# Kernel optimization log

Hardware: AMD Instinct MI355X
Metric: run time of the kernel (lower is better)

The kernel has to match this reference:

```python
import jax, jax.numpy as jnp
import numpy as np

B, N, D, DEG = 64, 128, 64, 16  # graphs, nodes/graph, emb_dim, degree


def setup_inputs() -> dict:
    key = jax.random.key(0)
    k1, k2 = jax.random.split(key)
    # ring-lattice edges per graph: node i -> (i+k) % N, k=1..DEG (no self loops, no duplicates)
    src_local = jnp.repeat(jnp.arange(N, dtype=jnp.int32), DEG)            # [N*DEG]
    dst_local = (src_local + jnp.tile(jnp.arange(1, DEG + 1, dtype=jnp.int32), N)) % N
    offsets = (jnp.arange(B, dtype=jnp.int32) * N)[:, None]                 # [B,1]
    src = (src_local[None, :] + offsets).reshape(-1)                        # [B*N*DEG]
    dst = (dst_local[None, :] + offsets).reshape(-1)
    edge_index = jnp.stack([src, dst], axis=0)                              # [2, E]
    batch_vec = jnp.repeat(jnp.arange(B, dtype=jnp.int32), N)               # [B*N]
    edge_attr = jax.random.normal(k1, (B * N * DEG, D), dtype=jnp.float32)
    emb_table = jax.random.normal(k2, (3, D), dtype=jnp.float32)
    emb_table = emb_table.at[0].set(0.0)  # padding_idx=0 -> zero row
    return {"edge_attr": edge_attr, "emb_table": emb_table,
            "edge_index": edge_index, "batch_vec": batch_vec,
            "num_graphs": B, "max_nodes": N}


def reference(edge_attr, emb_table, edge_index, batch_vec, num_graphs, max_nodes):
    total_nodes = batch_vec.shape[0]
    ones = jnp.ones((total_nodes,), dtype=jnp.int32)
    counts = jax.ops.segment_sum(ones, batch_vec, num_segments=num_graphs)  # nodes per graph
    offsets = jnp.cumsum(counts) - counts                                   # exclusive cumsum
    local = jnp.arange(total_nodes, dtype=jnp.int32) - offsets[batch_vec]   # node idx within graph

    g = batch_vec[edge_index[0]]            # graph id per edge
    si = local[edge_index[0]]
    di = local[edge_index[1]]

    # to_dense_adj(edge_index, batch, edge_attr): scatter-add edge features -> [B, N, N, D]
    edge_dense = jnp.zeros((num_graphs, max_nodes, max_nodes, edge_attr.shape[-1]),
                           dtype=edge_attr.dtype)
    edge_dense = edge_dense.at[g, si, di].add(edge_attr)

    # A = 2 - dense(edge val 2, self-loop val 1, else 0) -> 0 edge, 1 diag, 2 disconnected/pad
    A = jnp.full((num_graphs, max_nodes, max_nodes), 2, dtype=jnp.int32)
    A = A.at[g, si, di].add(-2)
    A = A.at[batch_vec, local, local].add(-1)

    # Embedding(3, D, padding_idx=0): row 0 is zeros
    emb = emb_table[A] * (A != 0)[..., None].astype(emb_table.dtype)
    return edge_dense + emb
```

## Files before the change

kernel.cpp:

```cpp
#include <hip/hip_runtime.h>


__global__ void prep_kernel(const int* __restrict__ batch, int* __restrict__ ws,
                            int TN, int B) {
    extern __shared__ int cnt[];
    for (int i = threadIdx.x; i < B; i += blockDim.x) cnt[i] = 0;
    __syncthreads();
    for (int v = threadIdx.x; v < TN; v += blockDim.x)
        atomicAdd(&cnt[batch[v]], 1);
    __syncthreads();
    if (threadIdx.x == 0) {
        int acc = 0;
        for (int g = 0; g < B; ++g) {
            int c = cnt[g];
            ws[g]     = acc;
            ws[B + g] = c;
            acc += c;
        }
    }
}

__global__ void fill_kernel(float4* __restrict__ out, const float4* __restrict__ emb,
                            const int* __restrict__ counts, int N, int D4, int jPer) {
    int g  = blockIdx.z;
    int i  = blockIdx.y;
    int d4 = threadIdx.x % D4;
    int jj = threadIdx.x / D4;
    int j  = blockIdx.x * jPer + jj;
    if (j >= N) return;
    float4 v1 = emb[D4 + d4];
    float4 v2 = emb[2 * D4 + d4];
    bool diag = (j == i) && (i < counts[g]);
    float4 v = diag ? v1 : v2;
    size_t row = (size_t)(g * N + i);
    out[(row * N + j) * D4 + d4] = v;
}

__global__ void edge_kernel(const float4* __restrict__ attr, const int* __restrict__ eidx,
                            const int* __restrict__ batch, const int* __restrict__ offs,
                            float4* __restrict__ out, int E, int N, int D4) {
    int idx = blockIdx.x * blockDim.x + threadIdx.x;
    if (idx >= E * D4) return;
    int e  = idx / D4;
    int d4 = idx - e * D4;
    int s  = eidx[e];
    int d  = eidx[E + e];
    int g  = batch[s];
    int off = offs[g];
    int si = s - off;
    int di = d - off;
    float4 v = attr[(size_t)e * D4 + d4];
    out[(((size_t)g * N + si) * N + di) * D4 + d4] = v;
}

extern "C" void kernel_launch(void* const* d_in, const int* in_sizes, int n_in,
                              void* d_out, int out_size, void* d_ws, size_t ws_size,
                              hipStream_t stream) {
    const float* edge_attr  = (const float*)d_in[0];
    const float* emb_table  = (const float*)d_in[1];
    const int*   edge_index = (const int*)d_in[2];
    const int*   batch_vec  = (const int*)d_in[3];

    int D  = in_sizes[1] / 3;
    int E  = in_sizes[2] / 2;
    int TN = in_sizes[3];
    int D4 = D / 4;
    int N  = (int)((long long)out_size / ((long long)TN * (long long)D));
    int B  = TN / N;

    float* out = (float*)d_out;
    int*   ws  = (int*)d_ws;

    prep_kernel<<<1, 1024, (size_t)B * sizeof(int), stream>>>(batch_vec, ws, TN, B);

    int jPer = 256 / D4;
    dim3 fgrid((N + jPer - 1) / jPer, N, B);
    fill_kernel<<<fgrid, 256, 0, stream>>>((float4*)out, (const float4*)emb_table,
                                           ws + B, N, D4, jPer);

    long long eunits = (long long)E * D4;
    int eblocks = (int)((eunits + 255) / 256);
    edge_kernel<<<eblocks, 256, 0, stream>>>((const float4*)edge_attr, edge_index,
                                             batch_vec, ws, (float4*)out, E, N, D4);
}
```

Baseline: 70.21 us.

## Fuse background fill and edge scatter per row using CSR edge lists

After: 150.2 us. 2.14x slower.

```diff
diff --git a/kernel.cpp b/kernel.cpp
--- a/kernel.cpp
+++ b/kernel.cpp
@@ -1,4 +1,119 @@
 #include <hip/hip_runtime.h>
+
+
+
+__global__ void zero_kernel(int* __restrict__ ws, int beg, int end) {
+    int i = beg + blockIdx.x * blockDim.x + threadIdx.x;
+    int stride = gridDim.x * blockDim.x;
+    for (; i < end; i += stride) ws[i] = 0;
+}
+
+__global__ void hist_kernel(const int* __restrict__ batch, const int* __restrict__ eidx,
+                            int* __restrict__ ws, int B, int TN, int E) {
+    int* counts = ws + B;
+    int* rowcnt = ws + 2 * B + TN + 1;
+    int idx = blockIdx.x * blockDim.x + threadIdx.x;
+    int stride = gridDim.x * blockDim.x;
+    for (int v = idx; v < TN; v += stride) atomicAdd(&counts[batch[v]], 1);
+    for (int e = idx; e < E; e += stride) atomicAdd(&rowcnt[eidx[e]], 1);
+}
+
+__global__ __launch_bounds__(1024) void scan_kernel(int* __restrict__ ws, int B, int TN) {
+    int* offs   = ws;
+    int* counts = ws + B;
+    int* rowoff = ws + 2 * B;
+    int* rowcnt = ws + 2 * B + TN + 1;
+    __shared__ int part[1024];
+    int tid = threadIdx.x;
+    int nb  = (int)blockDim.x;
+    int chunk = (TN + nb - 1) / nb;
+    int s0 = tid * chunk;
+    int s1 = min(s0 + chunk, TN);
+    int sum = 0;
+    for (int r = s0; r < s1; ++r) sum += rowcnt[r];
+    part[tid] = sum;
+    __syncthreads();
+    for (int off = 1; off < nb; off <<= 1) {
+        int v = (tid >= off) ? part[tid - off] : 0;
+        __syncthreads();
+        if (tid >= off) part[tid] += v;
+        __syncthreads();
+    }
+    int excl = (tid == 0) ? 0 : part[tid - 1];
+    for (int r = s0; r < s1; ++r) { rowoff[r] = excl; excl += rowcnt[r]; }
+    if (s1 == TN) rowoff[TN] = excl;
+    if (tid == 0) {
+        int acc = 0;
+        for (int g = 0; g < B; ++g) { offs[g] = acc; acc += counts[g]; }
+    }
+}
+
+__global__ void scatter_kernel(const int* __restrict__ eidx, int* __restrict__ ws,
+                               int2* __restrict__ elist, int B, int TN, int E) {
+    const int* rowoff = ws + 2 * B;
+    int* rowcur = ws + 2 * B + 2 * TN + 1;
+    int idx = blockIdx.x * blockDim.x + threadIdx.x;
+    int stride = gridDim.x * blockDim.x;
+    for (int e = idx; e < E; e += stride) {
+        int s = eidx[e];
+        int pos = atomicAdd(&rowcur[s], 1);
+        elist[rowoff[s] + pos] = make_int2(eidx[E + e], e);
+    }
+}
+
+
+__global__ __launch_bounds__(256) void fused_kernel(
+        const float4* __restrict__ attr, const float4* __restrict__ emb,
+        const int2* __restrict__ elist, const int* __restrict__ ws,
+        float4* __restrict__ out, int B, int N, int D4, int lg) {
+    const int* offs   = ws;
+    const int* counts = ws + B;
+    const int* rowoff = ws + 2 * B;
+
+    int bid = blockIdx.x;
+    int g = bid / N;
+    int i = bid - g * N;
+    int cnt = counts[g];
+    int off = offs[g];
+    bool real = (i < cnt);
+    int kbeg = 0, kend = 0;
+    if (real) {
+        int s = off + i;
+        kbeg = rowoff[s];
+        kend = rowoff[s + 1];
+    }
+    int k = kend - kbeg;
+    if (k > 1024) k = 1024;
+
+    __shared__ int2 lds[1024];
+    for (int m = threadIdx.x; m < k; m += blockDim.x) {
+        int2 v = elist[kbeg + m];
+        lds[m] = make_int2(v.x - off, v.y);
+    }
+    __syncthreads();
+
+    int d4 = threadIdx.x & (D4 - 1);
+    int j0 = threadIdx.x >> lg;
+    int jStep = (int)blockDim.x >> lg;
+    float4 v1 = emb[D4 + d4];
+    float4 v2 = emb[2 * D4 + d4];
+    size_t outBase = (size_t)bid * ((size_t)N << lg);
+
+    for (int j = j0; j < N; j += jStep) {
+        float4 val = (real && j == i) ? v1 : v2;
+        out[outBase + ((size_t)j << lg) + d4] = val;
+    }
+    __syncthreads();
+
+    int units = k << lg;
+    for (int t = threadIdx.x; t < units; t += blockDim.x) {
+        int m  = t >> lg;
+        int dd = t & (D4 - 1);
+        int2 ed = lds[m];
+        float4 a = attr[((size_t)ed.y << lg) + dd];
+        out[outBase + ((size_t)ed.x << lg) + dd] = a;
+    }
+}
 
 
 __global__ void prep_kernel(const int* __restrict__ batch, int* __restrict__ ws,
@@ -13,9 +128,7 @@
         int acc = 0;
         for (int g = 0; g < B; ++g) {
             int c = cnt[g];
-            ws[g]     = acc;
-            ws[B + g] = c;
-            acc += c;
+            ws[g] = acc; ws[B + g] = c; acc += c;
         }
     }
 }
@@ -47,10 +160,8 @@
     int d  = eidx[E + e];
     int g  = batch[s];
     int off = offs[g];
-    int si = s - off;
-    int di = d - off;
-    float4 v = attr[(size_t)e * D4 + d4];
-    out[(((size_t)g * N + si) * N + di) * D4 + d4] = v;
+    out[(((size_t)g * N + (s - off)) * N + (d - off)) * D4 + d4] =
+        attr[(size_t)e * D4 + d4];
 }
 
 extern "C" void kernel_launch(void* const* d_in, const int* in_sizes, int n_in,
@@ -68,18 +179,37 @@
     int N  = (int)((long long)out_size / ((long long)TN * (long long)D));
     int B  = TN / N;
 
+    int lg = 0;
+    while ((1 << lg) < D4) ++lg;
+    bool pow2 = ((1 << lg) == D4) && (D4 >= 1) && (D4 <= 256) && (D % 4 == 0);
+
     float* out = (float*)d_out;
     int*   ws  = (int*)d_ws;
 
-    prep_kernel<<<1, 1024, (size_t)B * sizeof(int), stream>>>(batch_vec, ws, TN, B);
-
-    int jPer = 256 / D4;
-    dim3 fgrid((N + jPer - 1) / jPer, N, B);
-    fill_kernel<<<fgrid, 256, 0, stream>>>((float4*)out, (const float4*)emb_table,
-                                           ws + B, N, D4, jPer);
-
-    long long eunits = (long long)E * D4;
-    int eblocks = (int)((eunits + 255) / 256);
-    edge_kernel<<<eblocks, 256, 0, stream>>>((const float4*)edge_attr, edge_index,
-                                             batch_vec, ws, (float4*)out, E, N, D4);
-}
+    long long intHdr = 2LL * B + 3LL * TN + 1;
+    long long eoffInt = (intHdr + 1) & ~1LL;
+    long long needBytes = eoffInt * 4 + (long long)E * 8;
+
+    if (pow2 && (long long)ws_size >= needBytes) {
+        int2* elist = (int2*)(ws + eoffInt);
+        int zEnd = (int)intHdr;
+
+        zero_kernel<<<64, 256, 0, stream>>>(ws, B, zEnd);
+        hist_kernel<<<256, 256, 0, stream>>>(batch_vec, edge_index, ws, B, TN, E);
+        scan_kernel<<<1, 1024, 0, stream>>>(ws, B, TN);
+        scatter_kernel<<<256, 256, 0, stream>>>(edge_index, ws, elist, B, TN, E);
+        fused_kernel<<<B * N, 256, 0, stream>>>((const float4*)edge_attr,
+                                                (const float4*)emb_table, elist, ws,
+                                                (float4*)out, B, N, D4, lg);
+    } else {
+        prep_kernel<<<1, 1024, (size_t)B * sizeof(int), stream>>>(batch_vec, ws, TN, B);
+        int jPer = 256 / D4;
+        dim3 fgrid((N + jPer - 1) / jPer, N, B);
+        fill_kernel<<<fgrid, 256, 0, stream>>>((float4*)out, (const float4*)emb_table,
+                                               ws + B, N, D4, jPer);
+        long long eunits = (long long)E * D4;
+        int eblocks = (int)((eunits + 255) / 256);
+        edge_kernel<<<eblocks, 256, 0, stream>>>((const float4*)edge_attr, edge_index,
+                                                 batch_vec, ws, (float4*)out, E, N, D4);
+    }
+}
```

## Build edge bitmask to skip overwritten fill stores and merge fill with edge scatter

Applied to the files above, without the earlier changes.

New measurement: 75.43 us. 7.4% more time.

```diff
diff --git a/kernel.cpp b/kernel.cpp
--- a/kernel.cpp
+++ b/kernel.cpp
@@ -1,4 +1,81 @@
 #include <hip/hip_runtime.h>
+
+
+typedef float f4 __attribute__((ext_vector_type(4)));
+
+__global__ __launch_bounds__(256) void prep_zero_kernel(
+        const int* __restrict__ batch, int* __restrict__ offs,
+        f4* __restrict__ mask4, long long mask4N, int TN, int B) {
+    if (blockIdx.x == 0) {
+        __shared__ int cnt[1024];
+        for (int i = threadIdx.x; i < B; i += 256) cnt[i] = 0;
+        __syncthreads();
+        for (int v = threadIdx.x; v < TN; v += 256)
+            atomicAdd(&cnt[batch[v]], 1);
+        __syncthreads();
+        if (threadIdx.x == 0) {
+            int acc = 0;
+            for (int g = 0; g < B; ++g) { offs[g] = acc; acc += cnt[g]; }
+            offs[B] = acc;
+        }
+    } else {
+        long long idx = (long long)(blockIdx.x - 1) * 256 + threadIdx.x;
+        long long stride = (long long)(gridDim.x - 1) * 256;
+        f4 z = {0.f, 0.f, 0.f, 0.f};
+        for (; idx < mask4N; idx += stride) mask4[idx] = z;
+    }
+}
+
+__global__ void mask_build_kernel(const int* __restrict__ eidx,
+                                  const int* __restrict__ batch,
+                                  const int* __restrict__ offs,
+                                  unsigned* __restrict__ mask,
+                                  int E, int N, int lgN) {
+    int e = blockIdx.x * blockDim.x + threadIdx.x;
+    if (e >= E) return;
+    int s = eidx[e], d = eidx[E + e];
+    int g = batch[s];
+    int off = offs[g];
+    long long cell = (((long long)g << lgN) + (s - off)) * N + (d - off);
+    atomicOr(&mask[cell >> 5], 1u << ((int)cell & 31));
+}
+
+__global__ __launch_bounds__(256) void main_kernel(
+        const f4* __restrict__ attr, const f4* __restrict__ emb,
+        const int* __restrict__ eidx, const int* __restrict__ batch,
+        const int* __restrict__ offs, const unsigned* __restrict__ mask,
+        f4* __restrict__ out,
+        int E, int N, int D4, int lg, int lgN, int lgCPR, int eBlocks) {
+    int bid = blockIdx.x;
+    if (bid < eBlocks) {
+        long long idx = (long long)bid * 256 + threadIdx.x;
+        if (idx < ((long long)E << lg)) {
+            int e  = (int)(idx >> lg);
+            int d4 = (int)idx & (D4 - 1);
+            int s = eidx[e], d = eidx[E + e];
+            int g = batch[s];
+            int off = offs[g];
+            size_t row = ((size_t)g << lgN) + (s - off);
+            out[(row * N + (d - off)) * D4 + d4] = attr[((size_t)e << lg) + d4];
+        }
+    } else {
+        int fb   = bid - eBlocks;
+        int chunk = fb & ((1 << lgCPR) - 1);
+        int rowi  = fb >> lgCPR;
+        int i = rowi & (N - 1);
+        int g = rowi >> lgN;
+        int o0 = offs[g], o1 = offs[g + 1];
+        bool real = (i < o1 - o0);
+        int unit = (chunk << 8) + threadIdx.x;
+        int j  = unit >> lg;
+        int d4 = unit & (D4 - 1);
+        f4 v = (real && j == i) ? emb[D4 + d4] : emb[2 * D4 + d4];
+        long long cell = ((long long)rowi << lgN) + j;
+        unsigned bit = (mask[cell >> 5] >> ((int)cell & 31)) & 1u;
+        if (!bit)
+            out[((size_t)rowi << (lgN + lg)) + unit] = v;
+    }
+}
 
 
 __global__ void prep_kernel(const int* __restrict__ batch, int* __restrict__ ws,
@@ -13,14 +90,12 @@
         int acc = 0;
         for (int g = 0; g < B; ++g) {
             int c = cnt[g];
-            ws[g]     = acc;
-            ws[B + g] = c;
-            acc += c;
+            ws[g] = acc; ws[B + g] = c; acc += c;
         }
     }
 }
 
-__global__ void fill_kernel(float4* __restrict__ out, const float4* __restrict__ emb,
+__global__ void fill_kernel(f4* __restrict__ out, const f4* __restrict__ emb,
                             const int* __restrict__ counts, int N, int D4, int jPer) {
     int g  = blockIdx.z;
     int i  = blockIdx.y;
@@ -28,17 +103,17 @@
     int jj = threadIdx.x / D4;
     int j  = blockIdx.x * jPer + jj;
     if (j >= N) return;
-    float4 v1 = emb[D4 + d4];
-    float4 v2 = emb[2 * D4 + d4];
+    f4 v1 = emb[D4 + d4];
+    f4 v2 = emb[2 * D4 + d4];
     bool diag = (j == i) && (i < counts[g]);
-    float4 v = diag ? v1 : v2;
+    f4 v = diag ? v1 : v2;
     size_t row = (size_t)(g * N + i);
     out[(row * N + j) * D4 + d4] = v;
 }
 
-__global__ void edge_kernel(const float4* __restrict__ attr, const int* __restrict__ eidx,
+__global__ void edge_kernel(const f4* __restrict__ attr, const int* __restrict__ eidx,
                             const int* __restrict__ batch, const int* __restrict__ offs,
-                            float4* __restrict__ out, int E, int N, int D4) {
+                            f4* __restrict__ out, int E, int N, int D4) {
     int idx = blockIdx.x * blockDim.x + threadIdx.x;
     if (idx >= E * D4) return;
     int e  = idx / D4;
@@ -47,10 +122,8 @@
     int d  = eidx[E + e];
     int g  = batch[s];
     int off = offs[g];
-    int si = s - off;
-    int di = d - off;
-    float4 v = attr[(size_t)e * D4 + d4];
-    out[(((size_t)g * N + si) * N + di) * D4 + d4] = v;
+    out[(((size_t)g * N + (s - off)) * N + (d - off)) * D4 + d4] =
+        attr[(size_t)e * D4 + d4];
 }
 
 extern "C" void kernel_launch(void* const* d_in, const int* in_sizes, int n_in,
@@ -68,18 +141,51 @@
     int N  = (int)((long long)out_size / ((long long)TN * (long long)D));
     int B  = TN / N;
 
-    float* out = (float*)d_out;
-    int*   ws  = (int*)d_ws;
+    f4*  out = (f4*)d_out;
+    int* ws  = (int*)d_ws;
 
-    prep_kernel<<<1, 1024, (size_t)B * sizeof(int), stream>>>(batch_vec, ws, TN, B);
+    auto ispow2 = [](int x) { return x > 0 && (x & (x - 1)) == 0; };
+    int lg = 0;  while ((1 << lg) < D4) ++lg;
+    int lgN = 0; while ((1 << lgN) < N) ++lgN;
+    int unitsRow = N * D4;
+    int CPR = unitsRow >> 8;
+    int lgCPR = 0; while ((1 << lgCPR) < CPR) ++lgCPR;
 
-    int jPer = 256 / D4;
-    dim3 fgrid((N + jPer - 1) / jPer, N, B);
-    fill_kernel<<<fgrid, 256, 0, stream>>>((float4*)out, (const float4*)emb_table,
-                                           ws + B, N, D4, jPer);
+    long long maskWords = ((long long)TN * N) / 32;
+    int maskOff = ((B + 1 + 31) / 32) * 32;
+    long long needBytes = ((long long)maskOff + maskWords) * 4;
 
-    long long eunits = (long long)E * D4;
-    int eblocks = (int)((eunits + 255) / 256);
-    edge_kernel<<<eblocks, 256, 0, stream>>>((const float4*)edge_attr, edge_index,
-                                             batch_vec, ws, (float4*)out, E, N, D4);
+    bool fast = ispow2(D4) && D4 <= 256 && (D % 4 == 0) &&
+                ispow2(N) && unitsRow >= 256 && (unitsRow & 255) == 0 &&
+                ispow2(CPR) && B <= 1024 &&
+                (((long long)TN * N) % 128 == 0) &&
+                (long long)ws_size >= needBytes;
+
+    if (fast) {
+        int* offs = ws;
+        unsigned* mask = (unsigned*)(ws + maskOff);
+        long long mask4N = maskWords / 4;
+
+        int zBlocks = (int)((mask4N + 255) / 256);
+        prep_zero_kernel<<<1 + zBlocks, 256, 0, stream>>>(batch_vec, offs,
+                                                          (f4*)mask, mask4N, TN, B);
+        mask_build_kernel<<<(E + 255) / 256, 256, 0, stream>>>(edge_index, batch_vec,
+                                                               offs, mask, E, N, lgN);
+        long long eUnits = (long long)E << lg;
+        int eBlocks = (int)((eUnits + 255) / 256);
+        int fillBlocks = TN * CPR;
+        main_kernel<<<eBlocks + fillBlocks, 256, 0, stream>>>(
+            (const f4*)edge_attr, (const f4*)emb_table, edge_index, batch_vec,
+            offs, mask, out, E, N, D4, lg, lgN, lgCPR, eBlocks);
+    } else {
+        prep_kernel<<<1, 1024, (size_t)B * sizeof(int), stream>>>(batch_vec, ws, TN, B);
+        int jPer = 256 / D4;
+        dim3 fgrid((N + jPer - 1) / jPer, N, B);
+        fill_kernel<<<fgrid, 256, 0, stream>>>(out, (const f4*)emb_table,
+                                               ws + B, N, D4, jPer);
+        long long eunits = (long long)E * D4;
+        int eblocks = (int)((eunits + 255) / 256);
+        edge_kernel<<<eblocks, 256, 0, stream>>>((const f4*)edge_attr, edge_index,
+                                                 batch_vec, ws, out, E, N, D4);
+    }
 }
```

## Fold prep into flat fill kernel and move diagonal writes into edge kernel

Applied to the files above, without the earlier changes.

Result: faster. 65.55 us (-6.6%).

```diff
diff --git a/kernel.cpp b/kernel.cpp
--- a/kernel.cpp
+++ b/kernel.cpp
@@ -1,4 +1,58 @@
 #include <hip/hip_runtime.h>
+
+
+typedef float f4 __attribute__((ext_vector_type(4)));
+
+__global__ __launch_bounds__(256) void fillprep_kernel(
+        f4* __restrict__ out, const f4* __restrict__ emb,
+        const int* __restrict__ batch, int* __restrict__ offs,
+        int TN, int B, int D4, int fillBlocks) {
+    if ((int)blockIdx.x == fillBlocks) {
+        __shared__ int cnt[1024];
+        for (int i = threadIdx.x; i < B; i += 256) cnt[i] = 0;
+        __syncthreads();
+        for (int v = threadIdx.x; v < TN; v += 256)
+            atomicAdd(&cnt[batch[v]], 1);
+        __syncthreads();
+        if (threadIdx.x == 0) {
+            int acc = 0;
+            for (int g = 0; g < B; ++g) { offs[g] = acc; acc += cnt[g]; }
+            offs[B] = acc;
+        }
+        return;
+    }
+    size_t unit = ((size_t)blockIdx.x << 8) + threadIdx.x;
+    f4 v2 = emb[2 * D4 + (int)(unit & (D4 - 1))];
+    out[unit] = v2;
+}
+
+__global__ __launch_bounds__(256) void diagedge_kernel(
+        const f4* __restrict__ attr, const f4* __restrict__ emb,
+        const int* __restrict__ eidx, const int* __restrict__ batch,
+        const int* __restrict__ offs, f4* __restrict__ out,
+        int E, int N, int TN, int D4, int lg) {
+    long long idx = (long long)blockIdx.x * 256 + threadIdx.x;
+    long long dUnits = (long long)TN << lg;
+    if (idx < dUnits) {
+        int n  = (int)(idx >> lg);
+        int d4 = (int)idx & (D4 - 1);
+        int g = batch[n];
+        int i = n - offs[g];
+        size_t row = (size_t)(g * N + i);
+        out[(row * N + i) * D4 + d4] = emb[D4 + d4];
+        return;
+    }
+    idx -= dUnits;
+    if (idx < ((long long)E << lg)) {
+        int e  = (int)(idx >> lg);
+        int d4 = (int)idx & (D4 - 1);
+        int s = eidx[e], d = eidx[E + e];
+        int g = batch[s];
+        int off = offs[g];
+        size_t row = (size_t)(g * N + (s - off));
+        out[(row * N + (d - off)) * D4 + d4] = attr[((size_t)e << lg) + d4];
+    }
+}
 
 
 __global__ void prep_kernel(const int* __restrict__ batch, int* __restrict__ ws,
@@ -13,14 +67,12 @@
         int acc = 0;
         for (int g = 0; g < B; ++g) {
             int c = cnt[g];
-            ws[g]     = acc;
-            ws[B + g] = c;
-            acc += c;
+            ws[g] = acc; ws[B + g] = c; acc += c;
         }
     }
 }
 
-__global__ void fill_kernel(float4* __restrict__ out, const float4* __restrict__ emb,
+__global__ void fill_kernel(f4* __restrict__ out, const f4* __restrict__ emb,
                             const int* __restrict__ counts, int N, int D4, int jPer) {
     int g  = blockIdx.z;
     int i  = blockIdx.y;
@@ -28,17 +80,17 @@
     int jj = threadIdx.x / D4;
     int j  = blockIdx.x * jPer + jj;
     if (j >= N) return;
-    float4 v1 = emb[D4 + d4];
-    float4 v2 = emb[2 * D4 + d4];
+    f4 v1 = emb[D4 + d4];
+    f4 v2 = emb[2 * D4 + d4];
     bool diag = (j == i) && (i < counts[g]);
-    float4 v = diag ? v1 : v2;
+    f4 v = diag ? v1 : v2;
     size_t row = (size_t)(g * N + i);
     out[(row * N + j) * D4 + d4] = v;
 }
 
-__global__ void edge_kernel(const float4* __restrict__ attr, const int* __restrict__ eidx,
+__global__ void edge_kernel(const f4* __restrict__ attr, const int* __restrict__ eidx,
                             const int* __restrict__ batch, const int* __restrict__ offs,
-                            float4* __restrict__ out, int E, int N, int D4) {
+                            f4* __restrict__ out, int E, int N, int D4) {
     int idx = blockIdx.x * blockDim.x + threadIdx.x;
     if (idx >= E * D4) return;
     int e  = idx / D4;
@@ -47,10 +99,8 @@
     int d  = eidx[E + e];
     int g  = batch[s];
     int off = offs[g];
-    int si = s - off;
-    int di = d - off;
-    float4 v = attr[(size_t)e * D4 + d4];
-    out[(((size_t)g * N + si) * N + di) * D4 + d4] = v;
+    out[(((size_t)g * N + (s - off)) * N + (d - off)) * D4 + d4] =
+        attr[(size_t)e * D4 + d4];
 }
 
 extern "C" void kernel_launch(void* const* d_in, const int* in_sizes, int n_in,
@@ -68,18 +118,34 @@
     int N  = (int)((long long)out_size / ((long long)TN * (long long)D));
     int B  = TN / N;
 
-    float* out = (float*)d_out;
-    int*   ws  = (int*)d_ws;
+    f4*  out = (f4*)d_out;
+    int* ws  = (int*)d_ws;
 
-    prep_kernel<<<1, 1024, (size_t)B * sizeof(int), stream>>>(batch_vec, ws, TN, B);
+    long long total4 = (long long)out_size / 4;
+    bool pow2D4 = (D4 > 0) && ((D4 & (D4 - 1)) == 0) && D4 <= 256 && (D % 4 == 0);
+    bool fast = pow2D4 && (total4 % 256 == 0) && B <= 1024 &&
+                (long long)ws_size >= (long long)(B + 1) * 4;
 
-    int jPer = 256 / D4;
-    dim3 fgrid((N + jPer - 1) / jPer, N, B);
-    fill_kernel<<<fgrid, 256, 0, stream>>>((float4*)out, (const float4*)emb_table,
-                                           ws + B, N, D4, jPer);
+    if (fast) {
+        int lg = 0; while ((1 << lg) < D4) ++lg;
+        int fillBlocks = (int)(total4 >> 8);
+        fillprep_kernel<<<fillBlocks + 1, 256, 0, stream>>>(
+            out, (const f4*)emb_table, batch_vec, ws, TN, B, D4, fillBlocks);
 
-    long long eunits = (long long)E * D4;
-    int eblocks = (int)((eunits + 255) / 256);
-    edge_kernel<<<eblocks, 256, 0, stream>>>((const float4*)edge_attr, edge_index,
-                                             batch_vec, ws, (float4*)out, E, N, D4);
+        long long tUnits = ((long long)TN << lg) + ((long long)E << lg);
+        int bBlocks = (int)((tUnits + 255) / 256);
+        diagedge_kernel<<<bBlocks, 256, 0, stream>>>(
+            (const f4*)edge_attr, (const f4*)emb_table, edge_index, batch_vec,
+            ws, out, E, N, TN, D4, lg);
+    } else {
+        prep_kernel<<<1, 1024, (size_t)B * sizeof(int), stream>>>(batch_vec, ws, TN, B);
+        int jPer = 256 / D4; if (jPer < 1) jPer = 1;
+        dim3 fgrid((N + jPer - 1) / jPer, N, B);
+        fill_kernel<<<fgrid, 256, 0, stream>>>(out, (const f4*)emb_table,
+                                               ws + B, N, D4, jPer);
+        long long eunits = (long long)E * D4;
+        int eblocks = (int)((eunits + 255) / 256);
+        edge_kernel<<<eblocks, 256, 0, stream>>>((const f4*)edge_attr, edge_index,
+                                                 batch_vec, ws, out, E, N, D4);
+    }
 }
```
